# Kernel optimization log

Hardware: AMD Instinct MI355X
Metric: run time of the kernel (lower is better)

## Reference

```python
import jax, jax.numpy as jnp
import numpy as np

B, Q, K, D = 8, 2048, 2048, 512

def setup_inputs() -> dict:
    key = jax.random.key(0)
    k1, k2, k3, k4, k5 = jax.random.split(key, 5)
    return {
        "query": jax.random.normal(k1, (B, Q, D), dtype=jnp.float32),
        "key": jax.random.normal(k2, (B, K, D), dtype=jnp.float32),
        "value": jax.random.normal(k3, (B, K, D), dtype=jnp.float32),
        "key_mask": jax.random.randint(k4, (B, K), 0, 2, dtype=jnp.int32),
        "W": jax.random.normal(k5, (D, D), dtype=jnp.float32) / np.sqrt(D),
    }

def reference(query, key, value, key_mask, W):
    # bilinear score: s[b,q,k] = query[b,q,:] @ W @ key[b,k,:]
    scale = 1.0 / jnp.sqrt(jnp.asarray(query.shape[-1], query.dtype))
    qW = jnp.einsum('bqd,de->bqe', query, W)          # [B,Q,D]
    scores = jnp.einsum('bqe,bke->bqk', qW, key)      # [B,Q,K]
    scores = jnp.where(key_mask[:, None, :] == 0, jnp.asarray(-1e20, scores.dtype), scores) * scale
    dist = jax.nn.softmax(scores, axis=-1)            # [B,Q,K]
    context = jnp.einsum('bqk,bkd->bqd', dist, value) # [B,Q,D]
    return context, dist
```

## Files before the change

### kernel.cpp

```cpp
#include <hip/hip_runtime.h>
#include <stdint.h>

#define BB 8
#define QQ 2048
#define KK 2048
#define DD 512

typedef __bf16 bf16x8 __attribute__((ext_vector_type(8)));
typedef float f32x4 __attribute__((ext_vector_type(4)));

__device__ __forceinline__ unsigned short f2bf(float f) {
    union { float f; unsigned u; } x;
    x.f = f;
    unsigned r = x.u + 0x7fffu + ((x.u >> 16) & 1u);
    return (unsigned short)(r >> 16);
}

__global__ __launch_bounds__(256) void cvt_f32_bf16(const float* __restrict__ in,
                                                    unsigned short* __restrict__ out) {
    size_t i = ((size_t)blockIdx.x * 256 + threadIdx.x) * 4;
    float4 f = *(const float4*)(in + i);
    uint2 u;
    u.x = (unsigned)f2bf(f.x) | ((unsigned)f2bf(f.y) << 16);
    u.y = (unsigned)f2bf(f.z) | ((unsigned)f2bf(f.w) << 16);
    *(uint2*)(out + i) = u;
}

__global__ __launch_bounds__(256) void transpose_cvt(const float* __restrict__ in,
                                                     unsigned short* __restrict__ out,
                                                     int R, int C, long inB, long outB) {
    __shared__ float t[32][33];
    const float* ip = in + (size_t)blockIdx.z * inB;
    unsigned short* op = out + (size_t)blockIdx.z * outB;
    int x = threadIdx.x & 31, y0 = threadIdx.x >> 5;
    int c0 = blockIdx.x * 32, r0 = blockIdx.y * 32;
#pragma unroll
    for (int i = 0; i < 32; i += 8)
        t[y0 + i][x] = ip[(size_t)(r0 + y0 + i) * C + c0 + x];
    __syncthreads();
#pragma unroll
    for (int i = 0; i < 32; i += 8)
        op[(size_t)(c0 + y0 + i) * R + r0 + x] = f2bf(t[x][y0 + i]);
}

template <bool AF32, int OUTM>
__global__ __launch_bounds__(256) void gemm_bt(const void* __restrict__ Aall,
                                               const unsigned short* __restrict__ Ball,
                                               void* __restrict__ Call,
                                               const int* __restrict__ maskAll,
                                               int Kred, int lda, int ldb, int ldc,
                                               long aStride, long bStride, long cStride,
                                               int maskStride, float scale) {
    const int b = blockIdx.z;
    const int m0 = blockIdx.y * 128;
    const int n0 = blockIdx.x * 128;

    __shared__ unsigned short As[128 * 32];
    __shared__ unsigned short Bs[128 * 32];

    const int tid = threadIdx.x;
    const int lane = tid & 63, wave = tid >> 6;
    const int wm = wave >> 1, wn = wave & 1;
    const int lrow = lane & 15, quad = lane >> 4;

    const int r8 = tid >> 2, c8 = (tid & 3) * 8;
    const int r4 = tid >> 3, c4 = (tid & 7) * 4;

    const unsigned short* Bb = Ball + (size_t)b * bStride + (size_t)n0 * ldb;

    f32x4 acc[4][4];
#pragma unroll
    for (int mi = 0; mi < 4; mi++)
#pragma unroll
        for (int ni = 0; ni < 4; ni++)
            acc[mi][ni] = (f32x4){0.f, 0.f, 0.f, 0.f};

    for (int kk = 0; kk < Kred; kk += 32) {
        if constexpr (AF32) {
            const float* A = (const float*)Aall + (size_t)b * aStride + (size_t)m0 * lda + kk;
#pragma unroll
            for (int j = 0; j < 4; j++) {
                int row = j * 32 + r4;
                float4 f = *(const float4*)(A + (size_t)row * lda + c4);
                uint2 u;
                u.x = (unsigned)f2bf(f.x) | ((unsigned)f2bf(f.y) << 16);
                u.y = (unsigned)f2bf(f.z) | ((unsigned)f2bf(f.w) << 16);
                *(uint2*)&As[row * 32 + c4] = u;
            }
        } else {
            const unsigned short* A =
                (const unsigned short*)Aall + (size_t)b * aStride + (size_t)m0 * lda + kk;
#pragma unroll
            for (int j = 0; j < 2; j++) {
                int row = j * 64 + r8;
                *(uint4*)&As[row * 32 + c8] = *(const uint4*)(A + (size_t)row * lda + c8);
            }
        }
        {
            const unsigned short* Bp = Bb + kk;
#pragma unroll
            for (int j = 0; j < 2; j++) {
                int row = j * 64 + r8;
                *(uint4*)&Bs[row * 32 + c8] = *(const uint4*)(Bp + (size_t)row * ldb + c8);
            }
        }
        __syncthreads();

        bf16x8 af[4], bfr[4];
#pragma unroll
        for (int i = 0; i < 4; i++)
            af[i] = *(const bf16x8*)&As[(wm * 64 + i * 16 + lrow) * 32 + quad * 8];
#pragma unroll
        for (int i = 0; i < 4; i++)
            bfr[i] = *(const bf16x8*)&Bs[(wn * 64 + i * 16 + lrow) * 32 + quad * 8];

#pragma unroll
        for (int mi = 0; mi < 4; mi++)
#pragma unroll
            for (int ni = 0; ni < 4; ni++)
                acc[mi][ni] = __builtin_amdgcn_mfma_f32_16x16x32_bf16(af[mi], bfr[ni],
                                                                      acc[mi][ni], 0, 0, 0);
        __syncthreads();
    }

    const float mval = -1e20f * scale;
#pragma unroll
    for (int mi = 0; mi < 4; mi++) {
#pragma unroll
        for (int ni = 0; ni < 4; ni++) {
            int gm = m0 + wm * 64 + mi * 16 + quad * 4;
            int gn = n0 + wn * 64 + ni * 16 + lrow;
            if constexpr (OUTM == 0) {
                unsigned short* C = (unsigned short*)Call + (size_t)b * cStride;
#pragma unroll
                for (int r = 0; r < 4; r++)
                    C[(size_t)(gm + r) * ldc + gn] = f2bf(acc[mi][ni][r]);
            } else if constexpr (OUTM == 1) {
                float* C = (float*)Call + (size_t)b * cStride;
                const int* mk = maskAll + (size_t)b * maskStride;
                bool keep = mk[gn] != 0;
#pragma unroll
                for (int r = 0; r < 4; r++)
                    C[(size_t)(gm + r) * ldc + gn] = keep ? acc[mi][ni][r] * scale : mval;
            } else {
                float* C = (float*)Call + (size_t)b * cStride;
#pragma unroll
                for (int r = 0; r < 4; r++)
                    C[(size_t)(gm + r) * ldc + gn] = acc[mi][ni][r];
            }
        }
    }
}

__global__ __launch_bounds__(256) void softmax_rows(float* __restrict__ dist) {
    float* p = dist + (size_t)blockIdx.x * 2048;
    int tid = threadIdx.x;
    float4 a = *(float4*)(p + tid * 8);
    float4 b = *(float4*)(p + tid * 8 + 4);

    float m = fmaxf(fmaxf(fmaxf(a.x, a.y), fmaxf(a.z, a.w)),
                    fmaxf(fmaxf(b.x, b.y), fmaxf(b.z, b.w)));
#pragma unroll
    for (int off = 32; off > 0; off >>= 1) m = fmaxf(m, __shfl_down(m, off));

    __shared__ float red[8];
    if ((tid & 63) == 0) red[tid >> 6] = m;
    __syncthreads();
    m = fmaxf(fmaxf(red[0], red[1]), fmaxf(red[2], red[3]));

    a.x = __expf(a.x - m); a.y = __expf(a.y - m);
    a.z = __expf(a.z - m); a.w = __expf(a.w - m);
    b.x = __expf(b.x - m); b.y = __expf(b.y - m);
    b.z = __expf(b.z - m); b.w = __expf(b.w - m);

    float s = a.x + a.y + a.z + a.w + b.x + b.y + b.z + b.w;
#pragma unroll
    for (int off = 32; off > 0; off >>= 1) s += __shfl_down(s, off);
    if ((tid & 63) == 0) red[4 + (tid >> 6)] = s;
    __syncthreads();
    float inv = 1.0f / (red[4] + red[5] + red[6] + red[7]);

    a.x *= inv; a.y *= inv; a.z *= inv; a.w *= inv;
    b.x *= inv; b.y *= inv; b.z *= inv; b.w *= inv;
    *(float4*)(p + tid * 8) = a;
    *(float4*)(p + tid * 8 + 4) = b;
}

extern "C" void kernel_launch(void* const* d_in, const int* in_sizes, int n_in,
                              void* d_out, int out_size, void* d_ws, size_t ws_size,
                              hipStream_t stream) {
    const float* q    = (const float*)d_in[0];
    const float* k    = (const float*)d_in[1];
    const float* v    = (const float*)d_in[2];
    const int*   mask = (const int*)d_in[3];
    const float* W    = (const float*)d_in[4];

    float* ctx  = (float*)d_out;
    float* dist = ctx + (size_t)BB * QQ * DD;

    unsigned short* ws   = (unsigned short*)d_ws;
    unsigned short* Wt   = ws;
    unsigned short* Qbf  = Wt  + (size_t)DD * DD;
    unsigned short* Kbf  = Qbf + (size_t)BB * QQ * DD;
    unsigned short* Vt   = Kbf + (size_t)BB * KK * DD;
    unsigned short* qWbf = Vt  + (size_t)BB * DD * KK;

    const float scale = 0.044194173824159216f;

    transpose_cvt<<<dim3(DD / 32, DD / 32, 1), 256, 0, stream>>>(W, Wt, DD, DD, 0, 0);
    cvt_f32_bf16<<<dim3((BB * QQ * DD / 4) / 256), 256, 0, stream>>>(q, Qbf);
    cvt_f32_bf16<<<dim3((BB * KK * DD / 4) / 256), 256, 0, stream>>>(k, Kbf);
    transpose_cvt<<<dim3(DD / 32, KK / 32, BB), 256, 0, stream>>>(
        v, Vt, KK, DD, (long)KK * DD, (long)DD * KK);
    gemm_bt<false, 0><<<dim3(DD / 128, QQ / 128, BB), 256, 0, stream>>>(
        Qbf, Wt, qWbf, nullptr, DD, DD, DD, DD,
        (long)QQ * DD, 0, (long)QQ * DD, 0, 0.f);
    gemm_bt<false, 1><<<dim3(KK / 128, QQ / 128, BB), 256, 0, stream>>>(
        qWbf, Kbf, dist, mask, DD, DD, DD, KK,
        (long)QQ * DD, (long)KK * DD, (long)QQ * KK, KK, scale);
    softmax_rows<<<dim3(BB * QQ), 256, 0, stream>>>(dist);
    gemm_bt<true, 2><<<dim3(DD / 128, QQ / 128, BB), 256, 0, stream>>>(
        dist, Vt, ctx, nullptr, KK, KK, KK, DD,
        (long)QQ * KK, (long)DD * KK, (long)QQ * DD, 0, 0.f);
}
```

Before: 464.9 us.

## Switch to fp16 intermediates, store scores in half, use async global-to-LDS loads

Switches the matmul path from bf16 to fp16 MFMA. The score matrix is now kept as fp16 in the workspace: softmax reads half scores, writes the fp32 dist output, and also writes fp16 probabilities back in place for the PV GEMM, which no longer converts fp32 on the fly. The separate query conversion kernel is dropped by converting q inside the first GEMM, and bf16-operand tile loads use global_load_lds async copies. This cuts fp32 score traffic at the cost of fp16 precision for scores, with masked entries clamped to -60000 instead of -1e20.

```diff
diff --git a/kernel.cpp b/kernel.cpp
--- a/kernel.cpp
+++ b/kernel.cpp
@@ -6,24 +6,37 @@
 #define KK 2048
 #define DD 512
 
-typedef __bf16 bf16x8 __attribute__((ext_vector_type(8)));
+typedef _Float16 f16x8 __attribute__((ext_vector_type(8)));
 typedef float f32x4 __attribute__((ext_vector_type(4)));
 
-__device__ __forceinline__ unsigned short f2bf(float f) {
-    union { float f; unsigned u; } x;
-    x.f = f;
-    unsigned r = x.u + 0x7fffu + ((x.u >> 16) & 1u);
-    return (unsigned short)(r >> 16);
-}
-
-__global__ __launch_bounds__(256) void cvt_f32_bf16(const float* __restrict__ in,
-                                                    unsigned short* __restrict__ out) {
-    size_t i = ((size_t)blockIdx.x * 256 + threadIdx.x) * 4;
-    float4 f = *(const float4*)(in + i);
-    uint2 u;
-    u.x = (unsigned)f2bf(f.x) | ((unsigned)f2bf(f.y) << 16);
-    u.y = (unsigned)f2bf(f.z) | ((unsigned)f2bf(f.w) << 16);
-    *(uint2*)(out + i) = u;
+__device__ __forceinline__ unsigned short f2h(float f) {
+    union { _Float16 h; unsigned short u; } x;
+    x.h = (_Float16)f;
+    return x.u;
+}
+__device__ __forceinline__ float h2f(unsigned short u) {
+    union { unsigned short u; _Float16 h; } x;
+    x.u = u;
+    return (float)x.h;
+}
+
+__device__ __forceinline__ void async16(const unsigned short* g, unsigned short* l) {
+    __builtin_amdgcn_global_load_lds(
+        (const __attribute__((address_space(1))) unsigned int*)g,
+        (__attribute__((address_space(3))) unsigned int*)l, 16, 0, 0);
+}
+
+__global__ __launch_bounds__(256) void cvt_f32_f16(const float* __restrict__ in,
+                                                   unsigned short* __restrict__ out) {
+    size_t i = ((size_t)blockIdx.x * 256 + threadIdx.x) * 8;
+    float4 a = *(const float4*)(in + i);
+    float4 b = *(const float4*)(in + i + 4);
+    uint4 u;
+    u.x = (unsigned)f2h(a.x) | ((unsigned)f2h(a.y) << 16);
+    u.y = (unsigned)f2h(a.z) | ((unsigned)f2h(a.w) << 16);
+    u.z = (unsigned)f2h(b.x) | ((unsigned)f2h(b.y) << 16);
+    u.w = (unsigned)f2h(b.z) | ((unsigned)f2h(b.w) << 16);
+    *(uint4*)(out + i) = u;
 }
 
 __global__ __launch_bounds__(256) void transpose_cvt(const float* __restrict__ in,
@@ -40,7 +53,7 @@
     __syncthreads();
 #pragma unroll
     for (int i = 0; i < 32; i += 8)
-        op[(size_t)(c0 + y0 + i) * R + r0 + x] = f2bf(t[x][y0 + i]);
+        op[(size_t)(c0 + y0 + i) * R + r0 + x] = f2h(t[x][y0 + i]);
 }
 
 template <bool AF32, int OUTM>
@@ -63,10 +76,12 @@
     const int wm = wave >> 1, wn = wave & 1;
     const int lrow = lane & 15, quad = lane >> 4;
 
-    const int r8 = tid >> 2, c8 = (tid & 3) * 8;
-    const int r4 = tid >> 3, c4 = (tid & 7) * 4;
+    const int ar = tid >> 2, ac = (tid & 3) * 8;
+    const int fr = tid >> 3, fc = (tid & 7) * 4;
 
     const unsigned short* Bb = Ball + (size_t)b * bStride + (size_t)n0 * ldb;
+    unsigned short* AsW = As + wave * 512;
+    unsigned short* BsW = Bs + wave * 512;
 
     f32x4 acc[4][4];
 #pragma unroll
@@ -80,50 +95,45 @@
             const float* A = (const float*)Aall + (size_t)b * aStride + (size_t)m0 * lda + kk;
 #pragma unroll
             for (int j = 0; j < 4; j++) {
-                int row = j * 32 + r4;
-                float4 f = *(const float4*)(A + (size_t)row * lda + c4);
+                int row = j * 32 + fr;
+                float4 f = *(const float4*)(A + (size_t)row * lda + fc);
                 uint2 u;
-                u.x = (unsigned)f2bf(f.x) | ((unsigned)f2bf(f.y) << 16);
-                u.y = (unsigned)f2bf(f.z) | ((unsigned)f2bf(f.w) << 16);
-                *(uint2*)&As[row * 32 + c4] = u;
+                u.x = (unsigned)f2h(f.x) | ((unsigned)f2h(f.y) << 16);
+                u.y = (unsigned)f2h(f.z) | ((unsigned)f2h(f.w) << 16);
+                *(uint2*)&As[row * 32 + fc] = u;
             }
         } else {
             const unsigned short* A =
                 (const unsigned short*)Aall + (size_t)b * aStride + (size_t)m0 * lda + kk;
 #pragma unroll
-            for (int j = 0; j < 2; j++) {
-                int row = j * 64 + r8;
-                *(uint4*)&As[row * 32 + c8] = *(const uint4*)(A + (size_t)row * lda + c8);
-            }
+            for (int j = 0; j < 2; j++)
+                async16(A + (size_t)(j * 64 + ar) * lda + ac, AsW + j * 2048);
         }
         {
             const unsigned short* Bp = Bb + kk;
 #pragma unroll
-            for (int j = 0; j < 2; j++) {
-                int row = j * 64 + r8;
-                *(uint4*)&Bs[row * 32 + c8] = *(const uint4*)(Bp + (size_t)row * ldb + c8);
-            }
+            for (int j = 0; j < 2; j++)
+                async16(Bp + (size_t)(j * 64 + ar) * ldb + ac, BsW + j * 2048);
         }
         __syncthreads();
 
-        bf16x8 af[4], bfr[4];
+        f16x8 af[4], bfr[4];
 #pragma unroll
         for (int i = 0; i < 4; i++)
-            af[i] = *(const bf16x8*)&As[(wm * 64 + i * 16 + lrow) * 32 + quad * 8];
+            af[i] = *(const f16x8*)&As[(wm * 64 + i * 16 + lrow) * 32 + quad * 8];
 #pragma unroll
         for (int i = 0; i < 4; i++)
-            bfr[i] = *(const bf16x8*)&Bs[(wn * 64 + i * 16 + lrow) * 32 + quad * 8];
+            bfr[i] = *(const f16x8*)&Bs[(wn * 64 + i * 16 + lrow) * 32 + quad * 8];
 
 #pragma unroll
         for (int mi = 0; mi < 4; mi++)
 #pragma unroll
             for (int ni = 0; ni < 4; ni++)
-                acc[mi][ni] = __builtin_amdgcn_mfma_f32_16x16x32_bf16(af[mi], bfr[ni],
-                                                                      acc[mi][ni], 0, 0, 0);
+                acc[mi][ni] = __builtin_amdgcn_mfma_f32_16x16x32_f16(af[mi], bfr[ni],
+                                                                     acc[mi][ni], 0, 0, 0);
         __syncthreads();
     }
 
-    const float mval = -1e20f * scale;
 #pragma unroll
     for (int mi = 0; mi < 4; mi++) {
 #pragma unroll
@@ -134,14 +144,15 @@
                 unsigned short* C = (unsigned short*)Call + (size_t)b * cStride;
 #pragma unroll
                 for (int r = 0; r < 4; r++)
-                    C[(size_t)(gm + r) * ldc + gn] = f2bf(acc[mi][ni][r]);
+                    C[(size_t)(gm + r) * ldc + gn] = f2h(acc[mi][ni][r]);
             } else if constexpr (OUTM == 1) {
-                float* C = (float*)Call + (size_t)b * cStride;
+                unsigned short* C = (unsigned short*)Call + (size_t)b * cStride;
                 const int* mk = maskAll + (size_t)b * maskStride;
                 bool keep = mk[gn] != 0;
 #pragma unroll
                 for (int r = 0; r < 4; r++)
-                    C[(size_t)(gm + r) * ldc + gn] = keep ? acc[mi][ni][r] * scale : mval;
+                    C[(size_t)(gm + r) * ldc + gn] =
+                        keep ? f2h(acc[mi][ni][r] * scale) : f2h(-60000.f);
             } else {
                 float* C = (float*)Call + (size_t)b * cStride;
 #pragma unroll
@@ -152,14 +163,22 @@
     }
 }
 
-__global__ __launch_bounds__(256) void softmax_rows(float* __restrict__ dist) {
-    float* p = dist + (size_t)blockIdx.x * 2048;
+__global__ __launch_bounds__(256) void softmax_rows(unsigned short* __restrict__ sc,
+                                                    float* __restrict__ dist) {
+    unsigned short* sp = sc + (size_t)blockIdx.x * 2048;
+    float* dp = dist + (size_t)blockIdx.x * 2048;
     int tid = threadIdx.x;
-    float4 a = *(float4*)(p + tid * 8);
-    float4 b = *(float4*)(p + tid * 8 + 4);
-
-    float m = fmaxf(fmaxf(fmaxf(a.x, a.y), fmaxf(a.z, a.w)),
-                    fmaxf(fmaxf(b.x, b.y), fmaxf(b.z, b.w)));
+
+    uint4 u = *(uint4*)(sp + tid * 8);
+    float x[8];
+    x[0] = h2f((unsigned short)(u.x & 0xffff)); x[1] = h2f((unsigned short)(u.x >> 16));
+    x[2] = h2f((unsigned short)(u.y & 0xffff)); x[3] = h2f((unsigned short)(u.y >> 16));
+    x[4] = h2f((unsigned short)(u.z & 0xffff)); x[5] = h2f((unsigned short)(u.z >> 16));
+    x[6] = h2f((unsigned short)(u.w & 0xffff)); x[7] = h2f((unsigned short)(u.w >> 16));
+
+    float m = x[0];
+#pragma unroll
+    for (int i = 1; i < 8; i++) m = fmaxf(m, x[i]);
 #pragma unroll
     for (int off = 32; off > 0; off >>= 1) m = fmaxf(m, __shfl_down(m, off));
 
@@ -168,22 +187,29 @@
     __syncthreads();
     m = fmaxf(fmaxf(red[0], red[1]), fmaxf(red[2], red[3]));
 
-    a.x = __expf(a.x - m); a.y = __expf(a.y - m);
-    a.z = __expf(a.z - m); a.w = __expf(a.w - m);
-    b.x = __expf(b.x - m); b.y = __expf(b.y - m);
-    b.z = __expf(b.z - m); b.w = __expf(b.w - m);
-
-    float s = a.x + a.y + a.z + a.w + b.x + b.y + b.z + b.w;
+    float s = 0.f;
+#pragma unroll
+    for (int i = 0; i < 8; i++) { x[i] = __expf(x[i] - m); s += x[i]; }
 #pragma unroll
     for (int off = 32; off > 0; off >>= 1) s += __shfl_down(s, off);
     if ((tid & 63) == 0) red[4 + (tid >> 6)] = s;
     __syncthreads();
     float inv = 1.0f / (red[4] + red[5] + red[6] + red[7]);
 
-    a.x *= inv; a.y *= inv; a.z *= inv; a.w *= inv;
-    b.x *= inv; b.y *= inv; b.z *= inv; b.w *= inv;
-    *(float4*)(p + tid * 8) = a;
-    *(float4*)(p + tid * 8 + 4) = b;
+#pragma unroll
+    for (int i = 0; i < 8; i++) x[i] *= inv;
+
+    float4 o0 = {x[0], x[1], x[2], x[3]};
+    float4 o1 = {x[4], x[5], x[6], x[7]};
+    *(float4*)(dp + tid * 8) = o0;
+    *(float4*)(dp + tid * 8 + 4) = o1;
+
+    uint4 v;
+    v.x = (unsigned)f2h(x[0]) | ((unsigned)f2h(x[1]) << 16);
+    v.y = (unsigned)f2h(x[2]) | ((unsigned)f2h(x[3]) << 16);
+    v.z = (unsigned)f2h(x[4]) | ((unsigned)f2h(x[5]) << 16);
+    v.w = (unsigned)f2h(x[6]) | ((unsigned)f2h(x[7]) << 16);
+    *(uint4*)(sp + tid * 8) = v;
 }
 
 extern "C" void kernel_launch(void* const* d_in, const int* in_sizes, int n_in,
@@ -198,28 +224,27 @@
     float* ctx  = (float*)d_out;
     float* dist = ctx + (size_t)BB * QQ * DD;
 
-    unsigned short* ws   = (unsigned short*)d_ws;
-    unsigned short* Wt   = ws;
-    unsigned short* Qbf  = Wt  + (size_t)DD * DD;
-    unsigned short* Kbf  = Qbf + (size_t)BB * QQ * DD;
-    unsigned short* Vt   = Kbf + (size_t)BB * KK * DD;
-    unsigned short* qWbf = Vt  + (size_t)BB * DD * KK;
+    unsigned short* ws  = (unsigned short*)d_ws;
+    unsigned short* Wt  = ws;
+    unsigned short* Kh  = Wt + (size_t)DD * DD;
+    unsigned short* Vt  = Kh + (size_t)BB * KK * DD;
+    unsigned short* qWh = Vt + (size_t)BB * DD * KK;
+    unsigned short* Sc  = qWh + (size_t)BB * QQ * DD;
 
     const float scale = 0.044194173824159216f;
 
     transpose_cvt<<<dim3(DD / 32, DD / 32, 1), 256, 0, stream>>>(W, Wt, DD, DD, 0, 0);
-    cvt_f32_bf16<<<dim3((BB * QQ * DD / 4) / 256), 256, 0, stream>>>(q, Qbf);
-    cvt_f32_bf16<<<dim3((BB * KK * DD / 4) / 256), 256, 0, stream>>>(k, Kbf);
+    cvt_f32_f16<<<dim3((BB * KK * DD / 8) / 256), 256, 0, stream>>>(k, Kh);
     transpose_cvt<<<dim3(DD / 32, KK / 32, BB), 256, 0, stream>>>(
         v, Vt, KK, DD, (long)KK * DD, (long)DD * KK);
-    gemm_bt<false, 0><<<dim3(DD / 128, QQ / 128, BB), 256, 0, stream>>>(
-        Qbf, Wt, qWbf, nullptr, DD, DD, DD, DD,
+    gemm_bt<true, 0><<<dim3(DD / 128, QQ / 128, BB), 256, 0, stream>>>(
+        q, Wt, qWh, nullptr, DD, DD, DD, DD,
         (long)QQ * DD, 0, (long)QQ * DD, 0, 0.f);
     gemm_bt<false, 1><<<dim3(KK / 128, QQ / 128, BB), 256, 0, stream>>>(
-        qWbf, Kbf, dist, mask, DD, DD, DD, KK,
+        qWh, Kh, Sc, mask, DD, DD, DD, KK,
         (long)QQ * DD, (long)KK * DD, (long)QQ * KK, KK, scale);
-    softmax_rows<<<dim3(BB * QQ), 256, 0, stream>>>(dist);
-    gemm_bt<true, 2><<<dim3(DD / 128, QQ / 128, BB), 256, 0, stream>>>(
-        dist, Vt, ctx, nullptr, KK, KK, KK, DD,
+    softmax_rows<<<dim3(BB * QQ), 256, 0, stream>>>(Sc, dist);
+    gemm_bt<false, 2><<<dim3(DD / 128, QQ / 128, BB), 256, 0, stream>>>(
+        Sc, Vt, ctx, nullptr, KK, KK, KK, DD,
         (long)QQ * KK, (long)DD * KK, (long)QQ * DD, 0, 0.f);
 }
```

Measured after the change: 425.1 us. -8.6%, faster.
